# Performance work log

Measured on AMD Instinct MI355X. Metric: run time of the kernel, lower is better.

## Reference

```python
import jax, jax.numpy as jnp
import numpy as np

N_NODES = 50000
N_REL = 4
N_EDGES = 250000
IN_F, HID_F, OUT_F = 512, 512, 256


def setup_inputs() -> dict:
    key = jax.random.key(0)
    ks = jax.random.split(key, 9)
    x = jax.random.normal(ks[0], (N_NODES, IN_F), dtype=jnp.float32)
    edge_src = jax.random.randint(ks[1], (N_REL, N_EDGES), 0, N_NODES, dtype=jnp.int64)
    edge_dst = jax.random.randint(ks[2], (N_REL, N_EDGES), 0, N_NODES, dtype=jnp.int64)
    s1 = 1.0 / np.sqrt(IN_F)
    s2 = 1.0 / np.sqrt(HID_F)
    Wself1 = jax.random.normal(ks[3], (N_REL, IN_F, HID_F), dtype=jnp.float32) * s1
    Wneigh1 = jax.random.normal(ks[4], (N_REL, IN_F, HID_F), dtype=jnp.float32) * s1
    b1 = jnp.zeros((N_REL, HID_F), dtype=jnp.float32)
    Wself2 = jax.random.normal(ks[5], (N_REL, HID_F, OUT_F), dtype=jnp.float32) * s2
    Wneigh2 = jax.random.normal(ks[6], (N_REL, HID_F, OUT_F), dtype=jnp.float32) * s2
    b2 = jnp.zeros((N_REL, OUT_F), dtype=jnp.float32)
    return {"x": x, "Wself1": Wself1, "Wneigh1": Wneigh1, "b1": b1,
            "Wself2": Wself2, "Wneigh2": Wneigh2, "b2": b2,
            "edge_src": edge_src, "edge_dst": edge_dst}


def _hetero_sage_layer(h, Wself, Wneigh, b, edge_src, edge_dst):
    """HeteroGraphConv(sum) over per-relation SAGEConv(mean) layers.

    DGL SAGEConv(mean): out_r = h @ W_self_r + mean_in_neigh(h) @ W_neigh_r + b_r;
    zero-in-degree nodes get a zero neighbor term (divide by max(deg,1)).
    """
    n = h.shape[0]
    out = jnp.zeros((n, Wself.shape[-1]), dtype=h.dtype)
    for r in range(Wself.shape[0]):  # small fixed number of relations
        src, dst = edge_src[r], edge_dst[r]
        deg = jax.ops.segment_sum(jnp.ones(src.shape, dtype=h.dtype), dst, num_segments=n)
        neigh_sum = jax.ops.segment_sum(h[src], dst, num_segments=n)  # [n, d]
        neigh = neigh_sum / jnp.maximum(deg, 1.0)[:, None]
        out = out + h @ Wself[r] + neigh @ Wneigh[r] + b[r]
    return out


def reference(x, Wself1, Wneigh1, b1, Wself2, Wneigh2, b2, edge_src, edge_dst):
    h = _hetero_sage_layer(x, Wself1, Wneigh1, b1, edge_src, edge_dst)
    h = jax.nn.relu(h)
    return _hetero_sage_layer(h, Wself2, Wneigh2, b2, edge_src, edge_dst)
```

## Files before the change

kernel.cpp:

```cpp
#include <hip/hip_runtime.h>
#include <stdint.h>

#define NNODES 50000
#define NREL 4
#define INF 512
#define HIDF 512
#define OUTF 256
#define NEDGES 250000
#define KCAT 2560
#define N2 1280
#define SCANB 49

typedef unsigned short u16;
typedef u16 u16x4 __attribute__((ext_vector_type(4)));
typedef u16 u16x8 __attribute__((ext_vector_type(8)));
typedef __bf16 bf16x8 __attribute__((ext_vector_type(8)));
typedef float f32x4 __attribute__((ext_vector_type(4)));

__device__ __forceinline__ float bf2f(u16 b) {
    unsigned u = ((unsigned)b) << 16;
    return __builtin_bit_cast(float, u);
}
__device__ __forceinline__ u16 f2bf(float f) {
    unsigned u = __builtin_bit_cast(unsigned, f);
    u = (u + 0x7fffu + ((u >> 16) & 1u)) >> 16;
    return (u16)u;
}

#define GLOAD_LDS16(gsrc, ldst)                                                  \
    __builtin_amdgcn_global_load_lds(                                            \
        (__attribute__((address_space(1))) void*)(gsrc),                         \
        (__attribute__((address_space(3))) void*)(ldst), 16, 0, 0)


__global__ void cast_bf16_kernel(const float* __restrict__ in, u16* __restrict__ out, long total) {
    long i = ((long)blockIdx.x * blockDim.x + threadIdx.x) * 8;
    long stride = (long)gridDim.x * blockDim.x * 8;
    for (; i + 7 < total; i += stride) {
        float4 v0 = *(const float4*)(in + i);
        float4 v1 = *(const float4*)(in + i + 4);
        u16x8 o;
        o[0] = f2bf(v0.x); o[1] = f2bf(v0.y); o[2] = f2bf(v0.z); o[3] = f2bf(v0.w);
        o[4] = f2bf(v1.x); o[5] = f2bf(v1.y); o[6] = f2bf(v1.z); o[7] = f2bf(v1.w);
        *(u16x8*)(out + i) = o;
    }
}

__global__ __launch_bounds__(256) void prep_w_kernel(
    const float* __restrict__ Ws1, const float* __restrict__ Wn1,
    const float* __restrict__ Ws2, const float* __restrict__ Wn2,
    u16* __restrict__ WT1, u16* __restrict__ WT2) {
    __shared__ float tile[64][65];
    int bid = blockIdx.x;
    int l = threadIdx.x & 63, wv = threadIdx.x >> 6;
    if (bid < 320) {
        int s = bid >> 6, r = bid & 63, kt = r >> 3, nt = r & 7;
        int n0 = nt * 64 + l;
        for (int i = 0; i < 16; ++i) {
            int kl = wv + i * 4;
            int k = kt * 64 + kl;
            float v;
            if (s == 0) {
                v = Ws1[(size_t)k * HIDF + n0] + Ws1[((size_t)512 + k) * HIDF + n0] +
                    Ws1[((size_t)1024 + k) * HIDF + n0] + Ws1[((size_t)1536 + k) * HIDF + n0];
            } else {
                v = Wn1[((size_t)(s - 1) * 512 + k) * HIDF + n0];
            }
            tile[kl][l] = v;
        }
        __syncthreads();
        for (int i = 0; i < 16; ++i) {
            int nl = wv + i * 4;
            WT1[(size_t)(nt * 64 + nl) * KCAT + s * 512 + kt * 64 + l] = f2bf(tile[l][nl]);
        }
    } else {
        int b = bid - 320;
        int nt = b >> 3, kt = b & 7;
        int n0 = nt * 64 + l;
        int s = n0 >> 8, nn = n0 & 255;
        for (int i = 0; i < 16; ++i) {
            int kl = wv + i * 4;
            int k = kt * 64 + kl;
            float v;
            if (s == 0) {
                v = Ws2[(size_t)k * OUTF + nn] + Ws2[((size_t)512 + k) * OUTF + nn] +
                    Ws2[((size_t)1024 + k) * OUTF + nn] + Ws2[((size_t)1536 + k) * OUTF + nn];
            } else {
                v = Wn2[((size_t)(s - 1) * 512 + k) * OUTF + nn];
            }
            tile[kl][l] = v;
        }
        __syncthreads();
        for (int i = 0; i < 16; ++i) {
            int nl = wv + i * 4;
            WT2[(size_t)(nt * 64 + nl) * 512 + kt * 64 + l] = f2bf(tile[l][nl]);
        }
    }
}

__global__ void prep_bias_kernel(const float* __restrict__ b1, const float* __restrict__ b2,
                                 float* __restrict__ b1s, float* __restrict__ b2e) {
    int t = blockIdx.x * 1024 + threadIdx.x;
    if (t < HIDF) b1s[t] = b1[t] + b1[HIDF + t] + b1[2 * HIDF + t] + b1[3 * HIDF + t];
    int i = t - 512;
    if (i >= 0 && i < N2)
        b2e[i] = (i < OUTF) ? (b2[i] + b2[OUTF + i] + b2[2 * OUTF + i] + b2[3 * OUTF + i]) : 0.f;
}


__global__ void hist_kernel(const int* __restrict__ dst, int* __restrict__ deg) {
    int r = blockIdx.y;
    int i = blockIdx.x * blockDim.x + threadIdx.x;
    if (i < NEDGES) atomicAdd(&deg[r * NNODES + dst[r * NEDGES + i]], 1);
}

__global__ __launch_bounds__(1024) void scan1_kernel(const int* __restrict__ deg,
                                                     int* __restrict__ rp, int* __restrict__ bsum) {
    int rel = blockIdx.x / SCANB, blk = blockIdx.x % SCANB;
    int i = blk * 1024 + threadIdx.x;
    int v = (i < NNODES) ? deg[rel * NNODES + i] : 0;
    __shared__ int wsum[16];
    int lane = threadIdx.x & 63, wid = threadIdx.x >> 6;
    int x = v;
#pragma unroll
    for (int off = 1; off < 64; off <<= 1) {
        int o = __shfl_up(x, off);
        if (lane >= off) x += o;
    }
    if (lane == 63) wsum[wid] = x;
    __syncthreads();
    if (wid == 0) {
        int s = (lane < 16) ? wsum[lane] : 0;
#pragma unroll
        for (int off = 1; off < 16; off <<= 1) {
            int o = __shfl_up(s, off);
            if (lane >= off) s += o;
        }
        if (lane < 16) wsum[lane] = s;
    }
    __syncthreads();
    int excl = (wid > 0 ? wsum[wid - 1] : 0) + x - v;
    if (i < NNODES) rp[rel * (NNODES + 1) + i] = excl;
    if (threadIdx.x == 1023) bsum[blockIdx.x] = excl + v;
}

__global__ void scan2_kernel(const int* __restrict__ bsum, int* __restrict__ bofs) {
    int r = threadIdx.x >> 6, lane = threadIdx.x & 63;
    int v = (lane < SCANB) ? bsum[r * SCANB + lane] : 0;
    int x = v;
#pragma unroll
    for (int off = 1; off < 64; off <<= 1) {
        int o = __shfl_up(x, off);
        if (lane >= off) x += o;
    }
    if (lane < SCANB) bofs[r * SCANB + lane] = x - v;
}

__global__ __launch_bounds__(1024) void scan3_kernel(int* __restrict__ rp, int* __restrict__ cur,
                                                     const int* __restrict__ bofs) {
    int rel = blockIdx.x / SCANB, blk = blockIdx.x % SCANB;
    int i = blk * 1024 + threadIdx.x;
    if (i < NNODES) {
        int v = rp[rel * (NNODES + 1) + i] + bofs[rel * SCANB + blk];
        rp[rel * (NNODES + 1) + i] = v;
        cur[rel * NNODES + i] = v;
        if (i == 0) rp[rel * (NNODES + 1) + NNODES] = NEDGES;
    }
}

__global__ void fill_kernel(const int* __restrict__ esrc, const int* __restrict__ edst,
                            int* __restrict__ cur, int* __restrict__ col) {
    int r = blockIdx.y;
    int i = blockIdx.x * blockDim.x + threadIdx.x;
    if (i < NEDGES) {
        int d = edst[r * NEDGES + i];
        int pos = atomicAdd(&cur[r * NNODES + d], 1);
        col[r * NEDGES + pos] = esrc[r * NEDGES + i];
    }
}


__global__ __launch_bounds__(256) void aggregate_kernel(const u16* __restrict__ src,
                                                        const int* __restrict__ rp,
                                                        const int* __restrict__ col,
                                                        u16* __restrict__ out) {
    int node = blockIdx.x * 4 + (threadIdx.x >> 6);
    int rel = blockIdx.y;
    if (node >= NNODES) return;
    const int* r = rp + rel * (NNODES + 1);
    const int* cl = col + rel * NEDGES;
    int l = threadIdx.x & 63;
    int p0 = r[node], p1 = r[node + 1];
    int d = p1 - p0;
    float scale = (d > 0) ? 1.0f / (float)d : 1.0f;
    float acc[8] = {0.f, 0.f, 0.f, 0.f, 0.f, 0.f, 0.f, 0.f};
    const u16* srcl = src + l * 8;
    for (int base = 0; base < d; base += 64) {
        int ci = p0 + base + l;
        int myc = cl[ci < p1 ? ci : (p1 - 1)];
        int lim = d - base;
        if (lim > 64) lim = 64;
        for (int e = 0; e < lim; e += 8) {
            int idx[8]; float wgt[8];
#pragma unroll
            for (int j = 0; j < 8; ++j) {
                int ee = e + j;
                int lane = (ee < lim) ? ee : e;
                idx[j] = __builtin_amdgcn_readlane(myc, lane);
                wgt[j] = (ee < lim) ? scale : 0.0f;
            }
            u16x8 v[8];
#pragma unroll
            for (int j = 0; j < 8; ++j) v[j] = *(const u16x8*)(srcl + (size_t)idx[j] * 512);
#pragma unroll
            for (int j = 0; j < 8; ++j)
#pragma unroll
                for (int f = 0; f < 8; ++f) acc[f] += wgt[j] * bf2f(v[j][f]);
        }
    }
    u16x8 o;
#pragma unroll
    for (int j = 0; j < 8; ++j) o[j] = f2bf(acc[j]);
    *(u16x8*)(out + ((size_t)rel * NNODES + node) * 512 + l * 8) = o;
}


__global__ __launch_bounds__(256) void aggregate2_kernel(const u16* __restrict__ P,
                                                         const int* __restrict__ rp,
                                                         const int* __restrict__ col,
                                                         float* __restrict__ out) {
    int node = blockIdx.x * 4 + (threadIdx.x >> 6);
    if (node >= NNODES) return;
    int l = threadIdx.x & 63;
    u16x4 sv = *(const u16x4*)(P + (size_t)node * N2 + l * 4);
    float a0 = bf2f(sv[0]), a1 = bf2f(sv[1]), a2 = bf2f(sv[2]), a3 = bf2f(sv[3]);
#pragma unroll
    for (int r = 0; r < NREL; ++r) {
        const int* rpn = rp + r * (NNODES + 1);
        const int* cl = col + r * NEDGES;
        int p0 = rpn[node], p1 = rpn[node + 1];
        int d = p1 - p0;
        if (d <= 0) continue;
        float scale = 1.0f / (float)d;
        const u16* base = P + 256 + r * 256 + (size_t)l * 4;
        for (int b = 0; b < d; b += 64) {
            int ci = p0 + b + l;
            int myc = cl[ci < p1 ? ci : (p1 - 1)];
            int lim = d - b;
            if (lim > 64) lim = 64;
            for (int e = 0; e < lim; e += 8) {
                int idx[8]; float wgt[8];
#pragma unroll
                for (int j = 0; j < 8; ++j) {
                    int ee = e + j;
                    idx[j] = __builtin_amdgcn_readlane(myc, (ee < lim) ? ee : e);
                    wgt[j] = (ee < lim) ? scale : 0.0f;
                }
                u16x4 v[8];
#pragma unroll
                for (int j = 0; j < 8; ++j)
                    v[j] = *(const u16x4*)(base + (size_t)idx[j] * N2);
#pragma unroll
                for (int j = 0; j < 8; ++j) {
                    a0 += wgt[j] * bf2f(v[j][0]);
                    a1 += wgt[j] * bf2f(v[j][1]);
                    a2 += wgt[j] * bf2f(v[j][2]);
                    a3 += wgt[j] * bf2f(v[j][3]);
                }
            }
        }
    }
    float4 o = {a0, a1, a2, a3};
    *(float4*)(out + (size_t)node * OUTF + l * 4) = o;
}


template <int N, int NPL, int OUTMODE>
__global__ __launch_bounds__(256, 4) void gemm_kernel(
    const u16* __restrict__ A0, const u16* __restrict__ A1, const u16* __restrict__ A2,
    const u16* __restrict__ A3, const u16* __restrict__ A4, const u16* __restrict__ WT,
    const float* __restrict__ bias, void* __restrict__ outp, int M) {
    __shared__ u16 ldsA[128 * 64];
    __shared__ u16 ldsB[128 * 64];
    const int t = threadIdx.x;
    const int w = t >> 6, l = t & 63;
    const int wr = w >> 1, wc = w & 1;
    constexpr int KTOT = NPL * 512;

    constexpr int ncol = N >> 7;
    const int nwg = gridDim.x * gridDim.y;
    const int orig = blockIdx.y * gridDim.x + blockIdx.x;
    const int q = nwg >> 3, rr = nwg & 7, xcd = orig & 7, loc = orig >> 3;
    const int v = (xcd < rr) ? xcd * (q + 1) + loc : rr * (q + 1) + (xcd - rr) * q + loc;
    const int rowBase = (v / ncol) * 128;
    const int colBase = (v % ncol) * 128;

    f32x4 acc[4][4] = {};

    const u16* const As[5] = {A0, A1, A2, A3, A4};
    const int sr = t >> 3;
    const int gp = t & 7;
    const int lr = l & 15, lg = l >> 4;

#pragma unroll
    for (int s = 0; s < NPL; ++s) {
        const u16* __restrict__ Asrc = As[s];
        for (int ts = 0; ts < 8; ++ts) {
            const int klocal = ts * 64;
            const int kglob = s * 512 + klocal;
#pragma unroll
            for (int c = 0; c < 4; ++c) {
                int r = c * 32 + sr;
                int gl = gp ^ (r & 7);
                int grow = rowBase + r;
                if (grow > M - 1) grow = M - 1;
                const u16* gsrc = Asrc + (size_t)grow * 512 + klocal + gl * 8;
                GLOAD_LDS16(gsrc, ldsA + (c * 2048 + w * 512));
            }
#pragma unroll
            for (int c = 0; c < 4; ++c) {
                int r = c * 32 + sr;
                int gl = gp ^ (r & 7);
                const u16* gsrc = WT + (size_t)(colBase + r) * KTOT + kglob + gl * 8;
                GLOAD_LDS16(gsrc, ldsB + (c * 2048 + w * 512));
            }
            __syncthreads();
#pragma unroll
            for (int kh = 0; kh < 2; ++kh) {
                bf16x8 av[4], bv[4];
#pragma unroll
                for (int m = 0; m < 4; ++m) {
                    int r = wr * 64 + m * 16 + lr;
                    int g = (kh * 4 + lg) ^ (r & 7);
                    av[m] = *(const bf16x8*)((const char*)ldsA + r * 128 + g * 16);
                }
#pragma unroll
                for (int n = 0; n < 4; ++n) {
                    int r = wc * 64 + n * 16 + lr;
                    int g = (kh * 4 + lg) ^ (r & 7);
                    bv[n] = *(const bf16x8*)((const char*)ldsB + r * 128 + g * 16);
                }
#pragma unroll
                for (int m = 0; m < 4; ++m)
#pragma unroll
                    for (int n = 0; n < 4; ++n)
                        acc[m][n] =
                            __builtin_amdgcn_mfma_f32_16x16x32_bf16(av[m], bv[n], acc[m][n], 0, 0, 0);
            }
            __syncthreads();
        }
    }

    const int lq = l >> 4;
#pragma unroll
    for (int m = 0; m < 4; ++m) {
#pragma unroll
        for (int n = 0; n < 4; ++n) {
#pragma unroll
            for (int j = 0; j < 4; ++j) {
                int row = rowBase + wr * 64 + m * 16 + lq * 4 + j;
                int colc = colBase + wc * 64 + n * 16 + lr;
                if (row < M) {
                    float vv = acc[m][n][j] + bias[colc];
                    if (OUTMODE == 0) vv = vv > 0.f ? vv : 0.f;
                    ((u16*)outp)[(size_t)row * N + colc] = f2bf(vv);
                }
            }
        }
    }
}


extern "C" void kernel_launch(void* const* d_in, const int* in_sizes, int n_in,
                              void* d_out, int out_size, void* d_ws, size_t ws_size,
                              hipStream_t stream) {
    const float* x = (const float*)d_in[0];
    const float* Wself1 = (const float*)d_in[1];
    const float* Wneigh1 = (const float*)d_in[2];
    const float* b1 = (const float*)d_in[3];
    const float* Wself2 = (const float*)d_in[4];
    const float* Wneigh2 = (const float*)d_in[5];
    const float* b2 = (const float*)d_in[6];
    const int* esrc = (const int*)d_in[7];
    const int* edst = (const int*)d_in[8];

    char* ws = (char*)d_ws;
    size_t off = 0;
    auto alloc = [&](size_t bytes) {
        char* p = ws + off;
        off += (bytes + 255) & ~(size_t)255;
        return p;
    };
    const size_t plane = (size_t)NNODES * 512;
    u16* xB = (u16*)alloc(plane * 2);
    u16* mB = (u16*)alloc(NREL * plane * 2);
    u16* h1B = (u16*)alloc(plane * 2);
    u16* WT1 = (u16*)alloc((size_t)HIDF * KCAT * 2);
    u16* WT2 = (u16*)alloc((size_t)N2 * 512 * 2);
    float* b1s = (float*)alloc(HIDF * 4);
    float* b2e = (float*)alloc(N2 * 4);
    int* deg = (int*)alloc((size_t)NREL * NNODES * 4);
    int* rp = (int*)alloc((size_t)NREL * (NNODES + 1) * 4);
    int* cur = (int*)alloc((size_t)NREL * NNODES * 4);
    int* col = (int*)alloc((size_t)NREL * NEDGES * 4);
    int* bsum = (int*)alloc((size_t)NREL * SCANB * 4);
    int* bofs = (int*)alloc((size_t)NREL * SCANB * 4);

    hipMemsetAsync(deg, 0, (size_t)NREL * NNODES * 4, stream);
    cast_bf16_kernel<<<12500, 256, 0, stream>>>(x, xB, (long)NNODES * INF);
    prep_w_kernel<<<480, 256, 0, stream>>>(Wself1, Wneigh1, Wself2, Wneigh2, WT1, WT2);
    prep_bias_kernel<<<2, 1024, 0, stream>>>(b1, b2, b1s, b2e);
    hist_kernel<<<dim3(977, 4), 256, 0, stream>>>(edst, deg);
    scan1_kernel<<<NREL * SCANB, 1024, 0, stream>>>(deg, rp, bsum);
    scan2_kernel<<<1, 256, 0, stream>>>(bsum, bofs);
    scan3_kernel<<<NREL * SCANB, 1024, 0, stream>>>(rp, cur, bofs);
    fill_kernel<<<dim3(977, 4), 256, 0, stream>>>(esrc, edst, cur, col);

    aggregate_kernel<<<dim3(12500, 4), 256, 0, stream>>>(xB, rp, col, mB);
    gemm_kernel<HIDF, 5, 0><<<dim3(4, 391), 256, 0, stream>>>(
        xB, mB, mB + plane, mB + 2 * plane, mB + 3 * plane, WT1, b1s, h1B, NNODES);

    u16* P = mB;
    gemm_kernel<N2, 1, 2><<<dim3(10, 391), 256, 0, stream>>>(
        h1B, h1B, h1B, h1B, h1B, WT2, b2e, P, NNODES);
    aggregate2_kernel<<<12500, 256, 0, stream>>>(P, rp, col, (float*)d_out);
}
```

Baseline: 795.9 us.

## Use 256x256 GEMM tiles with double-buffered LDS and concatenated A planes

```diff
diff --git a/kernel.cpp b/kernel.cpp
--- a/kernel.cpp
+++ b/kernel.cpp
@@ -276,98 +276,119 @@
 
 
 template <int N, int NPL, int OUTMODE>
-__global__ __launch_bounds__(256, 4) void gemm_kernel(
-    const u16* __restrict__ A0, const u16* __restrict__ A1, const u16* __restrict__ A2,
-    const u16* __restrict__ A3, const u16* __restrict__ A4, const u16* __restrict__ WT,
+__global__ __launch_bounds__(512, 2) void gemm256_kernel(
+    const u16* __restrict__ Acat, const u16* __restrict__ WT,
     const float* __restrict__ bias, void* __restrict__ outp, int M) {
-    __shared__ u16 ldsA[128 * 64];
-    __shared__ u16 ldsB[128 * 64];
+    constexpr int KTOT = NPL * 512;
+    constexpr int NT = KTOT / 64;
+    constexpr int ncol = N >> 8;
+    __shared__ u16 lds[2][2][256 * 64];
+
     const int t = threadIdx.x;
     const int w = t >> 6, l = t & 63;
-    const int wr = w >> 1, wc = w & 1;
-    constexpr int KTOT = NPL * 512;
-
-    constexpr int ncol = N >> 7;
+    const int wm = w >> 2, wn = w & 3;
+    const int lr = l & 15, lg = l >> 4;
+    const int sr = t >> 3, gp = t & 7;
+
     const int nwg = gridDim.x * gridDim.y;
     const int orig = blockIdx.y * gridDim.x + blockIdx.x;
     const int q = nwg >> 3, rr = nwg & 7, xcd = orig & 7, loc = orig >> 3;
     const int v = (xcd < rr) ? xcd * (q + 1) + loc : rr * (q + 1) + (xcd - rr) * q + loc;
-    const int rowBase = (v / ncol) * 128;
-    const int colBase = (v % ncol) * 128;
-
-    f32x4 acc[4][4] = {};
-
-    const u16* const As[5] = {A0, A1, A2, A3, A4};
-    const int sr = t >> 3;
-    const int gp = t & 7;
-    const int lr = l & 15, lg = l >> 4;
-
-#pragma unroll
-    for (int s = 0; s < NPL; ++s) {
-        const u16* __restrict__ Asrc = As[s];
-        for (int ts = 0; ts < 8; ++ts) {
-            const int klocal = ts * 64;
-            const int kglob = s * 512 + klocal;
-#pragma unroll
-            for (int c = 0; c < 4; ++c) {
-                int r = c * 32 + sr;
-                int gl = gp ^ (r & 7);
-                int grow = rowBase + r;
-                if (grow > M - 1) grow = M - 1;
-                const u16* gsrc = Asrc + (size_t)grow * 512 + klocal + gl * 8;
-                GLOAD_LDS16(gsrc, ldsA + (c * 2048 + w * 512));
-            }
-#pragma unroll
-            for (int c = 0; c < 4; ++c) {
-                int r = c * 32 + sr;
-                int gl = gp ^ (r & 7);
-                const u16* gsrc = WT + (size_t)(colBase + r) * KTOT + kglob + gl * 8;
-                GLOAD_LDS16(gsrc, ldsB + (c * 2048 + w * 512));
-            }
-            __syncthreads();
-#pragma unroll
-            for (int kh = 0; kh < 2; ++kh) {
-                bf16x8 av[4], bv[4];
-#pragma unroll
-                for (int m = 0; m < 4; ++m) {
-                    int r = wr * 64 + m * 16 + lr;
-                    int g = (kh * 4 + lg) ^ (r & 7);
-                    av[m] = *(const bf16x8*)((const char*)ldsA + r * 128 + g * 16);
+    const int rowBase = (v / ncol) * 256;
+    const int colBase = (v % ncol) * 256;
+
+    f32x4 acc[8][4] = {};
+    const size_t planeElems = (size_t)M * 512;
+
+    auto STAGE = [&](int d, int kt) {
+        const int s = kt >> 3;
+        const int kloc = (kt & 7) * 64;
+        const u16* Ab = Acat + (size_t)s * planeElems + kloc;
+        const u16* Bb = WT + kt * 64;
+#pragma unroll
+        for (int c = 0; c < 4; ++c) {
+            int rA = c * 64 + sr;
+            int glA = gp ^ (rA & 7);
+            int grow = rowBase + rA; if (grow > M - 1) grow = M - 1;
+            GLOAD_LDS16(Ab + (size_t)grow * 512 + glA * 8, &lds[d][0][c * 4096 + w * 512]);
+        }
+#pragma unroll
+        for (int c = 0; c < 4; ++c) {
+            int rB = c * 64 + sr;
+            int glB = gp ^ (rB & 7);
+            GLOAD_LDS16(Bb + (size_t)(colBase + rB) * KTOT + glB * 8,
+                        &lds[d][1][c * 4096 + w * 512]);
+        }
+    };
+
+    STAGE(0, 0);
+    int db = 0;
+    for (int kt = 0; kt < NT; ++kt) {
+        if (kt + 1 < NT) {
+            STAGE(db ^ 1, kt + 1);
+            asm volatile("s_waitcnt vmcnt(8)" ::: "memory");
+        } else {
+            asm volatile("s_waitcnt vmcnt(0)" ::: "memory");
+        }
+        __builtin_amdgcn_s_barrier();
+        __builtin_amdgcn_sched_barrier(0);
+        const u16* La = lds[db][0];
+        const u16* Lb = lds[db][1];
+#pragma unroll
+        for (int mh = 0; mh < 2; ++mh)
+#pragma unroll
+            for (int nh = 0; nh < 2; ++nh) {
+                bf16x8 av[4][2], bv[2][2];
+#pragma unroll
+                for (int mi = 0; mi < 4; ++mi) {
+                    int rA = wm * 128 + (mh * 4 + mi) * 16 + lr;
+#pragma unroll
+                    for (int kh = 0; kh < 2; ++kh) {
+                        int g = (kh * 4 + lg) ^ (rA & 7);
+                        av[mi][kh] = *(const bf16x8*)((const char*)La + rA * 128 + g * 16);
+                    }
                 }
 #pragma unroll
-                for (int n = 0; n < 4; ++n) {
-                    int r = wc * 64 + n * 16 + lr;
-                    int g = (kh * 4 + lg) ^ (r & 7);
-                    bv[n] = *(const bf16x8*)((const char*)ldsB + r * 128 + g * 16);
+                for (int ni = 0; ni < 2; ++ni) {
+                    int rB = wn * 64 + (nh * 2 + ni) * 16 + lr;
+#pragma unroll
+                    for (int kh = 0; kh < 2; ++kh) {
+                        int g = (kh * 4 + lg) ^ (rB & 7);
+                        bv[ni][kh] = *(const bf16x8*)((const char*)Lb + rB * 128 + g * 16);
+                    }
                 }
-#pragma unroll
-                for (int m = 0; m < 4; ++m)
-#pragma unroll
-                    for (int n = 0; n < 4; ++n)
-                        acc[m][n] =
-                            __builtin_amdgcn_mfma_f32_16x16x32_bf16(av[m], bv[n], acc[m][n], 0, 0, 0);
-            }
-            __syncthreads();
-        }
+                __builtin_amdgcn_s_setprio(1);
+#pragma unroll
+                for (int mi = 0; mi < 4; ++mi)
+#pragma unroll
+                    for (int ni = 0; ni < 2; ++ni)
+#pragma unroll
+                        for (int kh = 0; kh < 2; ++kh)
+                            acc[mh * 4 + mi][nh * 2 + ni] =
+                                __builtin_amdgcn_mfma_f32_16x16x32_bf16(
+                                    av[mi][kh], bv[ni][kh],
+                                    acc[mh * 4 + mi][nh * 2 + ni], 0, 0, 0);
+                __builtin_amdgcn_s_setprio(0);
+            }
+        __syncthreads();
+        db ^= 1;
     }
 
     const int lq = l >> 4;
 #pragma unroll
-    for (int m = 0; m < 4; ++m) {
-#pragma unroll
-        for (int n = 0; n < 4; ++n) {
+    for (int mf = 0; mf < 8; ++mf)
+#pragma unroll
+        for (int nf = 0; nf < 4; ++nf)
 #pragma unroll
             for (int j = 0; j < 4; ++j) {
-                int row = rowBase + wr * 64 + m * 16 + lq * 4 + j;
-                int colc = colBase + wc * 64 + n * 16 + lr;
+                int row = rowBase + wm * 128 + mf * 16 + lq * 4 + j;
+                int colc = colBase + wn * 64 + nf * 16 + lr;
                 if (row < M) {
-                    float vv = acc[m][n][j] + bias[colc];
+                    float vv = acc[mf][nf][j] + bias[colc];
                     if (OUTMODE == 0) vv = vv > 0.f ? vv : 0.f;
                     ((u16*)outp)[(size_t)row * N + colc] = f2bf(vv);
                 }
             }
-        }
-    }
 }
 
 
@@ -392,8 +413,9 @@
         return p;
     };
     const size_t plane = (size_t)NNODES * 512;
-    u16* xB = (u16*)alloc(plane * 2);
-    u16* mB = (u16*)alloc(NREL * plane * 2);
+    u16* Acat = (u16*)alloc(5 * plane * 2);
+    u16* xB = Acat;
+    u16* mB = Acat + plane;
     u16* h1B = (u16*)alloc(plane * 2);
     u16* WT1 = (u16*)alloc((size_t)HIDF * KCAT * 2);
     u16* WT2 = (u16*)alloc((size_t)N2 * 512 * 2);
@@ -417,11 +439,9 @@
     fill_kernel<<<dim3(977, 4), 256, 0, stream>>>(esrc, edst, cur, col);
 
     aggregate_kernel<<<dim3(12500, 4), 256, 0, stream>>>(xB, rp, col, mB);
-    gemm_kernel<HIDF, 5, 0><<<dim3(4, 391), 256, 0, stream>>>(
-        xB, mB, mB + plane, mB + 2 * plane, mB + 3 * plane, WT1, b1s, h1B, NNODES);
-
-    u16* P = mB;
-    gemm_kernel<N2, 1, 2><<<dim3(10, 391), 256, 0, stream>>>(
-        h1B, h1B, h1B, h1B, h1B, WT2, b2e, P, NNODES);
+    gemm256_kernel<HIDF, 5, 0><<<dim3(2, 196), 512, 0, stream>>>(Acat, WT1, b1s, h1B, NNODES);
+
+    u16* P = Acat;
+    gemm256_kernel<N2, 1, 2><<<dim3(5, 196), 512, 0, stream>>>(h1B, WT2, b2e, P, NNODES);
     aggregate2_kernel<<<12500, 256, 0, stream>>>(P, rp, col, (float*)d_out);
 }
```

Result: slower. 854.8 us (+7.4%).
